# Kernel tuning notes

Measured on AMD Instinct MI355X. Metric: run time of the kernel, lower is better.

## Reference

```python
import jax, jax.numpy as jnp
import numpy as np

IN_FEATURES = 212445
NODE_SIZES = [IN_FEATURES, 65536, 16384, 128]
N_CLASSES = 20
BATCH = 32


def setup_inputs() -> dict:
    key = jax.random.key(0)
    ks = jax.random.split(key, 16)
    inp = {
        "x": jax.random.normal(ks[0], (BATCH, IN_FEATURES), dtype=jnp.float32),
        "W0": jax.random.normal(ks[1], (32, 1), dtype=jnp.float32) * 0.1,
        "b0": jax.random.normal(ks[2], (32,), dtype=jnp.float32) * 0.1,
        "W1": jax.random.normal(ks[3], (64, 32), dtype=jnp.float32) * 0.1,
        "b1": jax.random.normal(ks[4], (64,), dtype=jnp.float32) * 0.1,
        "W2": jax.random.normal(ks[5], (128, 64), dtype=jnp.float32) * 0.1,
        "b2": jax.random.normal(ks[6], (128,), dtype=jnp.float32) * 0.1,
        "fc_w": jax.random.normal(ks[7], (N_CLASSES, 128 * 128), dtype=jnp.float32) * 0.01,
        "fc_b": jax.random.normal(ks[8], (N_CLASSES,), dtype=jnp.float32) * 0.01,
        # random-tree adjacency: each input node has one parent output node
        "parent0": jax.random.randint(ks[9], (NODE_SIZES[0],), 0, NODE_SIZES[1], dtype=jnp.int32),
        "parent1": jax.random.randint(ks[10], (NODE_SIZES[1],), 0, NODE_SIZES[2], dtype=jnp.int32),
        "parent2": jax.random.randint(ks[11], (NODE_SIZES[2],), 0, NODE_SIZES[3], dtype=jnp.int32),
    }
    return inp


def _fgl(z, parent, n_out, W, b):
    """FGL layer: tree-adjacency reduction over nodes + channel mix.
    z: [N, C_in, n_in] -> [N, C_out, n_out]
    """
    N, C, n_in = z.shape
    # segment-sum reduce input nodes into their parent output node
    zt = jnp.moveaxis(z, 2, 0).reshape(n_in, N * C)          # [n_in, N*C]
    s = jax.ops.segment_sum(zt, parent, num_segments=n_out)  # [n_out, N*C]
    s = jnp.moveaxis(s.reshape(n_out, N, C), 0, 2)           # [N, C_in, n_out]
    # channel mixing (weight-normed linear over channels, shared across nodes)
    return jnp.einsum("oc,ncj->noj", W, s) + b[None, :, None]


def reference(x, W0, b0, W1, b1, W2, b2, fc_w, fc_b, parent0, parent1, parent2):
    N = x.shape[0]
    z = x[:, None, :]                                   # [N, 1, in_features]
    z = _fgl(z, parent0, NODE_SIZES[1], W0, b0)         # [N, 32, 65536]
    z = _fgl(z, parent1, NODE_SIZES[2], W1, b1)         # [N, 64, 16384]
    z = _fgl(z, parent2, NODE_SIZES[3], W2, b2)         # [N, 128, 128]
    logits = z.reshape(N, -1) @ fc_w.T + fc_b           # [N, n_classes]
    return logits
```

## Files before the change

### kernel.cpp

```cpp
#include <hip/hip_runtime.h>

#define IN_FEATURES 212445
#define N1 65536
#define N2 16384
#define NCLS 20
#define BATCH 32
#define HIST_BLOCKS 16


__global__ __launch_bounds__(256) void k_setup(
    const float* __restrict__ W0, const float* __restrict__ b0,
    const float* __restrict__ W1, const float* __restrict__ b1,
    const float* __restrict__ W2,
    const int* __restrict__ p1, const int* __restrict__ p2,
    float* __restrict__ t3, int* __restrict__ hist,
    float* __restrict__ u2, float* __restrict__ v2, float* __restrict__ w2)
{
    int t = threadIdx.x;
    int b = blockIdx.x;
    if (b == 0) {
        __shared__ float su1[64], sv1[64];
        if (t < 64) {
            float a = 0.f, bb = 0.f;
            for (int c = 0; c < 32; ++c) {
                float w = W1[t * 32 + c];
                a  += w * W0[c];
                bb += w * b0[c];
            }
            su1[t] = a; sv1[t] = bb;
        }
        __syncthreads();
        if (t < 128) {
            float a = 0.f, bb = 0.f, c = 0.f;
            for (int j = 0; j < 64; ++j) {
                float w = W2[t * 64 + j];
                a  += w * su1[j];
                bb += w * sv1[j];
                c  += w * b1[j];
            }
            u2[t] = a; v2[t] = bb; w2[t] = c;
        }
    } else if (b == 1) {
        for (int s = t; s < BATCH * 128; s += 256) t3[s] = 0.f;
    } else {
        __shared__ int hA[128], hB[128];
        if (t < 128) { hA[t] = 0; hB[t] = 0; }
        __syncthreads();
        const int total = N1 + N2;
        const int stride = HIST_BLOCKS * 256;
        for (int idx = (b - 2) * 256 + t; idx < total; idx += stride) {
            if (idx < N1) atomicAdd(&hA[p2[p1[idx]]], 1);
            else          atomicAdd(&hB[p2[idx - N1]], 1);
        }
        __syncthreads();
        hist[(b - 2) * 256 + t] = (t < 128) ? hA[t] : hB[t - 128];
    }
}

__global__ __launch_bounds__(256) void k_t3(
    const float* __restrict__ x,
    const int* __restrict__ p0, const int* __restrict__ p1,
    const int* __restrict__ p2, float* __restrict__ t3)
{
    __shared__ float acc[BATCH * 128];
    int t = threadIdx.x;
    for (int s = t; s < BATCH * 128; s += 256) acc[s] = 0.f;
    __syncthreads();

    for (int i = blockIdx.x * 256 + t; i < IN_FEATURES; i += 256 * 256) {
        int m = p2[p1[p0[i]]];
        const float* xp = x + i;
        #pragma unroll
        for (int r = 0; r < BATCH; ++r) {
            atomicAdd(&acc[r * 128 + m], xp[r * IN_FEATURES]);
        }
    }
    __syncthreads();
    for (int s = t; s < BATCH * 128; s += 256)
        atomicAdd(&t3[s], acc[s]);
}

__global__ __launch_bounds__(128) void k_final(
    const float* __restrict__ fc_w, const float* __restrict__ fc_b,
    const float* __restrict__ b2,
    const float* __restrict__ u2, const float* __restrict__ v2,
    const float* __restrict__ w2,
    const int* __restrict__ hist, const float* __restrict__ t3,
    float* __restrict__ out)
{
    __shared__ float su[128], sv[128], sw[128], sb[128];
    __shared__ float sA[128], red[128];
    __shared__ float st3[BATCH * 129];
    __shared__ float sconst;
    int m = threadIdx.x;
    int cls = blockIdx.x;

    su[m] = u2[m]; sv[m] = v2[m]; sw[m] = w2[m]; sb[m] = b2[m];
    for (int s = m; s < BATCH * 128; s += 128) {
        int r = s >> 7, mm = s & 127;
        st3[r * 129 + mm] = t3[s];
    }
    int c2 = 0, cn2 = 0;
    #pragma unroll
    for (int h = 0; h < HIST_BLOCKS; ++h) {
        c2  += hist[h * 256 + m];
        cn2 += hist[h * 256 + 128 + m];
    }
    __syncthreads();

    const float* fw = fc_w + cls * 16384 + m;
    float Sa = 0.f, Sv = 0.f, Sw = 0.f, Sb = 0.f;
    #pragma unroll 4
    for (int o = 0; o < 128; ++o) {
        float w = fw[o * 128];
        Sa += w * su[o];
        Sv += w * sv[o];
        Sw += w * sw[o];
        Sb += w * sb[o];
    }
    sA[m] = Sa;
    red[m] = (float)c2 * Sv + (float)cn2 * Sw + Sb;
    __syncthreads();
    for (int s = 64; s > 0; s >>= 1) {
        if (m < s) red[m] += red[m + s];
        __syncthreads();
    }
    if (m == 0) sconst = red[0] + fc_b[cls];
    __syncthreads();

    int n = m >> 2, q = m & 3;
    const float* tr = st3 + n * 129 + q * 32;
    const float* ar = sA + q * 32;
    float s = 0.f;
    #pragma unroll
    for (int k = 0; k < 32; ++k) s += ar[k] * tr[k];
    red[m] = s;
    __syncthreads();
    if (q == 0)
        out[n * NCLS + cls] = sconst + red[m] + red[m + 1] + red[m + 2] + red[m + 3];
}

extern "C" void kernel_launch(void* const* d_in, const int* in_sizes, int n_in,
                              void* d_out, int out_size, void* d_ws, size_t ws_size,
                              hipStream_t stream)
{
    const float* x    = (const float*)d_in[0];
    const float* W0   = (const float*)d_in[1];
    const float* b0   = (const float*)d_in[2];
    const float* W1   = (const float*)d_in[3];
    const float* b1   = (const float*)d_in[4];
    const float* W2   = (const float*)d_in[5];
    const float* b2   = (const float*)d_in[6];
    const float* fc_w = (const float*)d_in[7];
    const float* fc_b = (const float*)d_in[8];
    const int*   p0   = (const int*)d_in[9];
    const int*   p1   = (const int*)d_in[10];
    const int*   p2   = (const int*)d_in[11];

    char* ws = (char*)d_ws;
    float* t3   = (float*)(ws + 0);
    int*   hist = (int*)(ws + 16384);
    float* u2   = (float*)(ws + 32768);
    float* v2   = (float*)(ws + 33280);
    float* w2   = (float*)(ws + 33792);

    k_setup<<<2 + HIST_BLOCKS, 256, 0, stream>>>(W0, b0, W1, b1, W2, p1, p2,
                                                 t3, hist, u2, v2, w2);
    k_t3<<<256, 256, 0, stream>>>(x, p0, p1, p2, t3);
    k_final<<<NCLS, 128, 0, stream>>>(fc_w, fc_b, b2, u2, v2, w2, hist, t3,
                                      (float*)d_out);
}
```

Baseline: 154.9 us.

## Precompute composed parent index and split t3 reduction by row and chunk

```diff
diff --git a/kernel.cpp b/kernel.cpp
--- a/kernel.cpp
+++ b/kernel.cpp
@@ -5,16 +5,22 @@
 #define N2 16384
 #define NCLS 20
 #define BATCH 32
-#define HIST_BLOCKS 16
+#define HIST_BLOCKS 32
+#define MCHUNK 1024
+#define MBLOCKS ((IN_FEATURES + MCHUNK - 1) / MCHUNK)
+#define TCHUNK 4096
+#define TCHUNKS ((IN_FEATURES + TCHUNK - 1) / TCHUNK)
 
 
 __global__ __launch_bounds__(256) void k_setup(
     const float* __restrict__ W0, const float* __restrict__ b0,
     const float* __restrict__ W1, const float* __restrict__ b1,
     const float* __restrict__ W2,
-    const int* __restrict__ p1, const int* __restrict__ p2,
+    const int* __restrict__ p0, const int* __restrict__ p1,
+    const int* __restrict__ p2,
     float* __restrict__ t3, int* __restrict__ hist,
-    float* __restrict__ u2, float* __restrict__ v2, float* __restrict__ w2)
+    float* __restrict__ u2, float* __restrict__ v2, float* __restrict__ w2,
+    int* __restrict__ midx)
 {
     int t = threadIdx.x;
     int b = blockIdx.x;
@@ -42,7 +48,7 @@
         }
     } else if (b == 1) {
         for (int s = t; s < BATCH * 128; s += 256) t3[s] = 0.f;
-    } else {
+    } else if (b < 2 + HIST_BLOCKS) {
         __shared__ int hA[128], hB[128];
         if (t < 128) { hA[t] = 0; hB[t] = 0; }
         __syncthreads();
@@ -54,33 +60,57 @@
         }
         __syncthreads();
         hist[(b - 2) * 256 + t] = (t < 128) ? hA[t] : hB[t - 128];
+    } else {
+        int mb = b - (2 + HIST_BLOCKS);
+        int base = mb * MCHUNK;
+        #pragma unroll
+        for (int u = 0; u < MCHUNK / 256; ++u) {
+            int i = base + u * 256 + t;
+            if (i < IN_FEATURES) midx[i] = p2[p1[p0[i]]];
+        }
     }
 }
 
 __global__ __launch_bounds__(256) void k_t3(
-    const float* __restrict__ x,
-    const int* __restrict__ p0, const int* __restrict__ p1,
-    const int* __restrict__ p2, float* __restrict__ t3)
-{
-    __shared__ float acc[BATCH * 128];
+    const float* __restrict__ x, const int* __restrict__ midx,
+    float* __restrict__ t3)
+{
+    __shared__ float hist[4 * 128];
     int t = threadIdx.x;
-    for (int s = t; s < BATCH * 128; s += 256) acc[s] = 0.f;
-    __syncthreads();
-
-    for (int i = blockIdx.x * 256 + t; i < IN_FEATURES; i += 256 * 256) {
-        int m = p2[p1[p0[i]]];
-        const float* xp = x + i;
-        #pragma unroll
-        for (int r = 0; r < BATCH; ++r) {
-            atomicAdd(&acc[r * 128 + m], xp[r * IN_FEATURES]);
-        }
-    }
-    __syncthreads();
-    for (int s = t; s < BATCH * 128; s += 256)
-        atomicAdd(&t3[s], acc[s]);
-}
-
-__global__ __launch_bounds__(128) void k_final(
+    for (int s = t; s < 512; s += 256) hist[s] = 0.f;
+    __syncthreads();
+
+    int row   = blockIdx.x & 31;
+    int chunk = blockIdx.x >> 5;
+    int base  = chunk * TCHUNK;
+    const float* xr = x + (size_t)row * IN_FEATURES;
+    float* hw = hist + (t >> 6) * 128;
+
+    if (base + TCHUNK <= IN_FEATURES) {
+        for (int k = 0; k < TCHUNK / 1024; ++k) {
+            float v[4]; int mi[4];
+            #pragma unroll
+            for (int u = 0; u < 4; ++u) {
+                int i = base + (k * 4 + u) * 256 + t;
+                v[u]  = xr[i];
+                mi[u] = midx[i];
+            }
+            #pragma unroll
+            for (int u = 0; u < 4; ++u)
+                atomicAdd(&hw[mi[u]], v[u]);
+        }
+    } else {
+        for (int i = base + t; i < IN_FEATURES; i += 256)
+            atomicAdd(&hw[midx[i]], xr[i]);
+    }
+    __syncthreads();
+    if (t < 128) {
+        float s = hist[t] + hist[128 + t] + hist[256 + t] + hist[384 + t];
+        atomicAdd(&t3[row * 128 + t], s);
+    }
+}
+
+__global__ __launch_bounds__(256) void k_final(
     const float* __restrict__ fc_w, const float* __restrict__ fc_b,
     const float* __restrict__ b2,
     const float* __restrict__ u2, const float* __restrict__ v2,
@@ -89,55 +119,63 @@
     float* __restrict__ out)
 {
     __shared__ float su[128], sv[128], sw[128], sb[128];
-    __shared__ float sA[128], red[128];
+    __shared__ float sA[128];
+    __shared__ float pA[256], pV[256], pW[256], pB[256];
+    __shared__ float red[256];
     __shared__ float st3[BATCH * 129];
     __shared__ float sconst;
-    int m = threadIdx.x;
+    int t = threadIdx.x;
+    int m = t & 127, h = t >> 7;
     int cls = blockIdx.x;
 
-    su[m] = u2[m]; sv[m] = v2[m]; sw[m] = w2[m]; sb[m] = b2[m];
-    for (int s = m; s < BATCH * 128; s += 128) {
-        int r = s >> 7, mm = s & 127;
-        st3[r * 129 + mm] = t3[s];
-    }
-    int c2 = 0, cn2 = 0;
-    #pragma unroll
-    for (int h = 0; h < HIST_BLOCKS; ++h) {
-        c2  += hist[h * 256 + m];
-        cn2 += hist[h * 256 + 128 + m];
-    }
+    if (h == 0) { su[m] = u2[m]; sv[m] = v2[m]; sw[m] = w2[m]; sb[m] = b2[m]; }
+    for (int s = t; s < BATCH * 128; s += 256)
+        st3[(s >> 7) * 129 + (s & 127)] = t3[s];
     __syncthreads();
 
     const float* fw = fc_w + cls * 16384 + m;
     float Sa = 0.f, Sv = 0.f, Sw = 0.f, Sb = 0.f;
-    #pragma unroll 4
-    for (int o = 0; o < 128; ++o) {
-        float w = fw[o * 128];
-        Sa += w * su[o];
-        Sv += w * sv[o];
-        Sw += w * sw[o];
-        Sb += w * sb[o];
-    }
-    sA[m] = Sa;
-    red[m] = (float)c2 * Sv + (float)cn2 * Sw + Sb;
-    __syncthreads();
-    for (int s = 64; s > 0; s >>= 1) {
-        if (m < s) red[m] += red[m + s];
-        __syncthreads();
-    }
-    if (m == 0) sconst = red[0] + fc_b[cls];
-    __syncthreads();
-
-    int n = m >> 2, q = m & 3;
-    const float* tr = st3 + n * 129 + q * 32;
-    const float* ar = sA + q * 32;
+    #pragma unroll 8
+    for (int o = h * 64; o < h * 64 + 64; ++o) {
+        float wv = fw[o * 128];
+        Sa += wv * su[o]; Sv += wv * sv[o]; Sw += wv * sw[o]; Sb += wv * sb[o];
+    }
+    pA[t] = Sa; pV[t] = Sv; pW[t] = Sw; pB[t] = Sb;
+    __syncthreads();
+    if (h == 0) {
+        Sa = pA[m] + pA[128 + m]; Sv = pV[m] + pV[128 + m];
+        Sw = pW[m] + pW[128 + m]; Sb = pB[m] + pB[128 + m];
+        int c2 = 0, cn2 = 0;
+        #pragma unroll
+        for (int hb = 0; hb < HIST_BLOCKS; ++hb) {
+            c2  += hist[hb * 256 + m];
+            cn2 += hist[hb * 256 + 128 + m];
+        }
+        sA[m] = Sa;
+        red[m] = (float)c2 * Sv + (float)cn2 * Sw + Sb;
+    }
+    __syncthreads();
+    for (int s2 = 64; s2 > 0; s2 >>= 1) {
+        if (t < s2) red[t] += red[t + s2];
+        __syncthreads();
+    }
+    if (t == 0) sconst = red[0] + fc_b[cls];
+    __syncthreads();
+
+    int n = t >> 3, oc = t & 7;
+    const float* tr = st3 + n * 129 + oc * 16;
+    const float* ar = sA + oc * 16;
     float s = 0.f;
     #pragma unroll
-    for (int k = 0; k < 32; ++k) s += ar[k] * tr[k];
-    red[m] = s;
-    __syncthreads();
-    if (q == 0)
-        out[n * NCLS + cls] = sconst + red[m] + red[m + 1] + red[m + 2] + red[m + 3];
+    for (int k = 0; k < 16; ++k) s += ar[k] * tr[k];
+    red[t] = s;
+    __syncthreads();
+    if (oc == 0) {
+        float tot = sconst;
+        #pragma unroll
+        for (int k = 0; k < 8; ++k) tot += red[t + k];
+        out[n * NCLS + cls] = tot;
+    }
 }
 
 extern "C" void kernel_launch(void* const* d_in, const int* in_sizes, int n_in,
@@ -160,13 +198,14 @@
     char* ws = (char*)d_ws;
     float* t3   = (float*)(ws + 0);
     int*   hist = (int*)(ws + 16384);
-    float* u2   = (float*)(ws + 32768);
-    float* v2   = (float*)(ws + 33280);
-    float* w2   = (float*)(ws + 33792);
-
-    k_setup<<<2 + HIST_BLOCKS, 256, 0, stream>>>(W0, b0, W1, b1, W2, p1, p2,
-                                                 t3, hist, u2, v2, w2);
-    k_t3<<<256, 256, 0, stream>>>(x, p0, p1, p2, t3);
-    k_final<<<NCLS, 128, 0, stream>>>(fc_w, fc_b, b2, u2, v2, w2, hist, t3,
+    float* u2   = (float*)(ws + 49152);
+    float* v2   = (float*)(ws + 49664);
+    float* w2   = (float*)(ws + 50176);
+    int*   midx = (int*)(ws + 51200);
+
+    k_setup<<<2 + HIST_BLOCKS + MBLOCKS, 256, 0, stream>>>(
+        W0, b0, W1, b1, W2, p0, p1, p2, t3, hist, u2, v2, w2, midx);
+    k_t3<<<BATCH * TCHUNKS, 256, 0, stream>>>(x, midx, t3);
+    k_final<<<NCLS, 256, 0, stream>>>(fc_w, fc_b, b2, u2, v2, w2, hist, t3,
                                       (float*)d_out);
 }
```

After: 136.6 us. 11.8% less time.

## Precompute composed leaf-to-root index map and fuse final reduction into main kernel

Applied to the files above, without the earlier changes.

```diff
diff --git a/kernel.cpp b/kernel.cpp
--- a/kernel.cpp
+++ b/kernel.cpp
@@ -1,143 +1,224 @@
 #include <hip/hip_runtime.h>
 
-#define IN_FEATURES 212445
+#define IF 212445
 #define N1 65536
 #define N2 16384
 #define NCLS 20
 #define BATCH 32
-#define HIST_BLOCKS 16
-
+#define HISTB 32
+#define MCHUNK 1024
+#define MBLK ((IF + MCHUNK - 1) / MCHUNK)
+#define TCHUNK 2048
+#define NCH ((IF + TCHUNK - 1) / TCHUNK)
+#define TOTALB (8 * NCH)
+
+#define OFF_T3   0
+#define OFF_DONE 16384
+#define OFF_HIST 16400
+#define OFF_A    49168
+#define OFF_SV   59408
+#define OFF_SW   69648
+#define OFF_CP   79888
+#define OFF_MIDX 79968
 
 __global__ __launch_bounds__(256) void k_setup(
     const float* __restrict__ W0, const float* __restrict__ b0,
     const float* __restrict__ W1, const float* __restrict__ b1,
-    const float* __restrict__ W2,
-    const int* __restrict__ p1, const int* __restrict__ p2,
-    float* __restrict__ t3, int* __restrict__ hist,
-    float* __restrict__ u2, float* __restrict__ v2, float* __restrict__ w2)
+    const float* __restrict__ W2, const float* __restrict__ b2,
+    const float* __restrict__ fc_w, const float* __restrict__ fc_b,
+    const int* __restrict__ p0, const int* __restrict__ p1,
+    const int* __restrict__ p2, char* __restrict__ ws)
 {
-    int t = threadIdx.x;
-    int b = blockIdx.x;
-    if (b == 0) {
+    int t = threadIdx.x, b = blockIdx.x;
+    float* t3   = (float*)(ws + OFF_T3);
+    int*   done = (int*)(ws + OFF_DONE);
+    int*   hist = (int*)(ws + OFF_HIST);
+    float* A    = (float*)(ws + OFF_A);
+    float* Sv   = (float*)(ws + OFF_SV);
+    float* Sw   = (float*)(ws + OFF_SW);
+    float* CP   = (float*)(ws + OFF_CP);
+    int*   midx = (int*)(ws + OFF_MIDX);
+
+    if (b < MBLK) {
+        int i = b * MCHUNK + 4 * t;
+        if (i + 3 < IF) {
+            int4 p = *(const int4*)(p0 + i);
+            int4 r;
+            r.x = p2[p1[p.x]]; r.y = p2[p1[p.y]];
+            r.z = p2[p1[p.z]]; r.w = p2[p1[p.w]];
+            *(int4*)(midx + i) = r;
+        } else {
+            for (int j = i; j < IF; ++j) midx[j] = p2[p1[p0[j]]];
+        }
+    } else if (b == MBLK) {
+        for (int s = t; s < BATCH * 128; s += 256) t3[s] = 0.f;
+        if (t == 0) *done = 0;
+    } else if (b < MBLK + 1 + HISTB) {
+        int hb = b - (MBLK + 1);
+        __shared__ int hA[128], hB[128];
+        if (t < 128) { hA[t] = 0; hB[t] = 0; }
+        __syncthreads();
+        const int total = N1 + N2;
+        for (int idx = hb * 256 + t; idx < total; idx += HISTB * 256) {
+            if (idx < N1) atomicAdd(&hA[p2[p1[idx]]], 1);
+            else          atomicAdd(&hB[p2[idx - N1]], 1);
+        }
+        __syncthreads();
+        hist[hb * 256 + t] = (t < 128) ? hA[t] : hB[t - 128];
+    } else {
+        int cls = b - (MBLK + 1 + HISTB);
         __shared__ float su1[64], sv1[64];
+        __shared__ float su2[128], sv2[128], sw2[128], sb2[128];
+        __shared__ float pA[256], pV[256], pW[256], pB[256];
         if (t < 64) {
             float a = 0.f, bb = 0.f;
             for (int c = 0; c < 32; ++c) {
                 float w = W1[t * 32 + c];
-                a  += w * W0[c];
-                bb += w * b0[c];
+                a += w * W0[c]; bb += w * b0[c];
             }
             su1[t] = a; sv1[t] = bb;
         }
+        if (t >= 128) sb2[t - 128] = b2[t - 128];
         __syncthreads();
         if (t < 128) {
             float a = 0.f, bb = 0.f, c = 0.f;
             for (int j = 0; j < 64; ++j) {
                 float w = W2[t * 64 + j];
-                a  += w * su1[j];
-                bb += w * sv1[j];
-                c  += w * b1[j];
+                a += w * su1[j]; bb += w * sv1[j]; c += w * b1[j];
             }
-            u2[t] = a; v2[t] = bb; w2[t] = c;
-        }
-    } else if (b == 1) {
-        for (int s = t; s < BATCH * 128; s += 256) t3[s] = 0.f;
-    } else {
-        __shared__ int hA[128], hB[128];
-        if (t < 128) { hA[t] = 0; hB[t] = 0; }
-        __syncthreads();
-        const int total = N1 + N2;
-        const int stride = HIST_BLOCKS * 256;
-        for (int idx = (b - 2) * 256 + t; idx < total; idx += stride) {
-            if (idx < N1) atomicAdd(&hA[p2[p1[idx]]], 1);
-            else          atomicAdd(&hB[p2[idx - N1]], 1);
-        }
-        __syncthreads();
-        hist[(b - 2) * 256 + t] = (t < 128) ? hA[t] : hB[t - 128];
+            su2[t] = a; sv2[t] = bb; sw2[t] = c;
+        }
+        __syncthreads();
+        int m = t & 127, h = t >> 7;
+        const float* fw = fc_w + cls * 16384 + m;
+        float Sa = 0.f, SvA = 0.f, SwA = 0.f, SbA = 0.f;
+        #pragma unroll 8
+        for (int o = h * 64; o < h * 64 + 64; ++o) {
+            float w = fw[o * 128];
+            Sa += w * su2[o]; SvA += w * sv2[o];
+            SwA += w * sw2[o]; SbA += w * sb2[o];
+        }
+        pA[t] = Sa; pV[t] = SvA; pW[t] = SwA; pB[t] = SbA;
+        __syncthreads();
+        if (t < 128) {
+            A [cls * 128 + t] = pA[t] + pA[t + 128];
+            Sv[cls * 128 + t] = pV[t] + pV[t + 128];
+            Sw[cls * 128 + t] = pW[t] + pW[t + 128];
+            pB[t] = pB[t] + pB[t + 128];
+        }
+        __syncthreads();
+        for (int s2 = 64; s2 > 0; s2 >>= 1) {
+            if (t < s2) pB[t] += pB[t + s2];
+            __syncthreads();
+        }
+        if (t == 0) CP[cls] = fc_b[cls] + pB[0];
     }
 }
 
-__global__ __launch_bounds__(256) void k_t3(
-    const float* __restrict__ x,
-    const int* __restrict__ p0, const int* __restrict__ p1,
-    const int* __restrict__ p2, float* __restrict__ t3)
-{
-    __shared__ float acc[BATCH * 128];
-    int t = threadIdx.x;
-    for (int s = t; s < BATCH * 128; s += 256) acc[s] = 0.f;
-    __syncthreads();
-
-    for (int i = blockIdx.x * 256 + t; i < IN_FEATURES; i += 256 * 256) {
-        int m = p2[p1[p0[i]]];
-        const float* xp = x + i;
-        #pragma unroll
-        for (int r = 0; r < BATCH; ++r) {
-            atomicAdd(&acc[r * 128 + m], xp[r * IN_FEATURES]);
-        }
-    }
-    __syncthreads();
-    for (int s = t; s < BATCH * 128; s += 256)
-        atomicAdd(&t3[s], acc[s]);
-}
-
-__global__ __launch_bounds__(128) void k_final(
-    const float* __restrict__ fc_w, const float* __restrict__ fc_b,
-    const float* __restrict__ b2,
-    const float* __restrict__ u2, const float* __restrict__ v2,
-    const float* __restrict__ w2,
-    const int* __restrict__ hist, const float* __restrict__ t3,
+__global__ __launch_bounds__(256) void k_main(
+    const float* __restrict__ x, char* __restrict__ ws,
     float* __restrict__ out)
 {
-    __shared__ float su[128], sv[128], sw[128], sb[128];
-    __shared__ float sA[128], red[128];
-    __shared__ float st3[BATCH * 129];
-    __shared__ float sconst;
-    int m = threadIdx.x;
-    int cls = blockIdx.x;
-
-    su[m] = u2[m]; sv[m] = v2[m]; sw[m] = w2[m]; sb[m] = b2[m];
-    for (int s = m; s < BATCH * 128; s += 128) {
-        int r = s >> 7, mm = s & 127;
-        st3[r * 129 + mm] = t3[s];
-    }
-    int c2 = 0, cn2 = 0;
+    __shared__ float smem[8192];
+    __shared__ int isLast;
+    int t = threadIdx.x;
+    float* t3   = (float*)(ws + OFF_T3);
+    int*   done = (int*)(ws + OFF_DONE);
+    const int*   hist = (const int*)(ws + OFF_HIST);
+    const float* A    = (const float*)(ws + OFF_A);
+    const float* Svt  = (const float*)(ws + OFF_SV);
+    const float* Swt  = (const float*)(ws + OFF_SW);
+    const float* CP   = (const float*)(ws + OFF_CP);
+    const int*   midx = (const int*)(ws + OFF_MIDX);
+
+    for (int s = t; s < 512; s += 256) smem[s] = 0.f;
+    __syncthreads();
+
+    int g = blockIdx.x & 7, chunk = blockIdx.x >> 3;
+    int r0 = g * 4, base = chunk * TCHUNK;
+    const float* x0 = x + (size_t)(r0 + 0) * IF;
+    const float* x1 = x + (size_t)(r0 + 1) * IF;
+    const float* x2 = x + (size_t)(r0 + 2) * IF;
+    const float* x3 = x + (size_t)(r0 + 3) * IF;
+    int iend = base + TCHUNK; if (iend > IF) iend = IF;
+
+    #pragma unroll 2
+    for (int i = base + t; i < iend; i += 256) {
+        int m = midx[i];
+        float v0 = x0[i], v1 = x1[i], v2 = x2[i], v3 = x3[i];
+        atomicAdd(&smem[      m], v0);
+        atomicAdd(&smem[128 + m], v1);
+        atomicAdd(&smem[256 + m], v2);
+        atomicAdd(&smem[384 + m], v3);
+    }
+    __syncthreads();
+    {
+        int s0 = t, s1 = t + 256;
+        atomicAdd(&t3[(r0 + (s0 >> 7)) * 128 + (s0 & 127)], smem[s0]);
+        atomicAdd(&t3[(r0 + (s1 >> 7)) * 128 + (s1 & 127)], smem[s1]);
+    }
+    __threadfence();
+    if (t == 0) isLast = (atomicAdd(done, 1) == TOTALB - 1) ? 1 : 0;
+    __syncthreads();
+    if (!isLast) return;
+    __threadfence();
+
+    float* st3   = smem;
+    float* sA    = smem + 4224;
+    float* c2f   = smem + 6784;
+    float* cnf   = smem + 6912;
+    float* cpart = smem + 7040;
+    float* scst  = smem + 7200;
+
     #pragma unroll
-    for (int h = 0; h < HIST_BLOCKS; ++h) {
-        c2  += hist[h * 256 + m];
-        cn2 += hist[h * 256 + 128 + m];
-    }
-    __syncthreads();
-
-    const float* fw = fc_w + cls * 16384 + m;
-    float Sa = 0.f, Sv = 0.f, Sw = 0.f, Sb = 0.f;
-    #pragma unroll 4
-    for (int o = 0; o < 128; ++o) {
-        float w = fw[o * 128];
-        Sa += w * su[o];
-        Sv += w * sv[o];
-        Sw += w * sw[o];
-        Sb += w * sb[o];
-    }
-    sA[m] = Sa;
-    red[m] = (float)c2 * Sv + (float)cn2 * Sw + Sb;
-    __syncthreads();
-    for (int s = 64; s > 0; s >>= 1) {
-        if (m < s) red[m] += red[m + s];
-        __syncthreads();
-    }
-    if (m == 0) sconst = red[0] + fc_b[cls];
-    __syncthreads();
-
-    int n = m >> 2, q = m & 3;
-    const float* tr = st3 + n * 129 + q * 32;
-    const float* ar = sA + q * 32;
-    float s = 0.f;
+    for (int k = 0; k < 16; ++k) {
+        int s = t + 256 * k;
+        float v = __hip_atomic_load(&t3[s], __ATOMIC_RELAXED,
+                                    __HIP_MEMORY_SCOPE_AGENT);
+        st3[(s & 127) * 33 + (s >> 7)] = v;
+    }
     #pragma unroll
-    for (int k = 0; k < 32; ++k) s += ar[k] * tr[k];
-    red[m] = s;
-    __syncthreads();
-    if (q == 0)
-        out[n * NCLS + cls] = sconst + red[m] + red[m + 1] + red[m + 2] + red[m + 3];
+    for (int k = 0; k < 10; ++k) {
+        int q = t + 256 * k;
+        sA[(q & 127) * 20 + (q >> 7)] = A[q];
+    }
+    {
+        int acc = 0;
+        #pragma unroll
+        for (int h = 0; h < HISTB; ++h) acc += hist[h * 256 + t];
+        if (t < 128) c2f[t] = (float)acc; else cnf[t - 128] = (float)acc;
+    }
+    __syncthreads();
+    if (t < 160) {
+        int cls = t >> 3, m0 = (t & 7) * 16;
+        const float* sv = Svt + cls * 128;
+        const float* sw = Swt + cls * 128;
+        float s = 0.f;
+        #pragma unroll
+        for (int m = m0; m < m0 + 16; ++m)
+            s += c2f[m] * sv[m] + cnf[m] * sw[m];
+        cpart[t] = s;
+    }
+    __syncthreads();
+    if (t < NCLS) {
+        float s = CP[t];
+        #pragma unroll
+        for (int k = 0; k < 8; ++k) s += cpart[t * 8 + k];
+        scst[t] = s;
+    }
+    __syncthreads();
+    #pragma unroll
+    for (int k = 0; k < 3; ++k) {
+        int p = t + 256 * k;
+        if (p < BATCH * NCLS) {
+            int n = p / NCLS, cls = p - n * NCLS;
+            float acc = scst[cls];
+            #pragma unroll 8
+            for (int m = 0; m < 128; ++m)
+                acc += sA[m * 20 + cls] * st3[m * 33 + n];
+            out[p] = acc;
+        }
+    }
 }
 
 extern "C" void kernel_launch(void* const* d_in, const int* in_sizes, int n_in,
@@ -157,16 +238,7 @@
     const int*   p1   = (const int*)d_in[10];
     const int*   p2   = (const int*)d_in[11];
 
-    char* ws = (char*)d_ws;
-    float* t3   = (float*)(ws + 0);
-    int*   hist = (int*)(ws + 16384);
-    float* u2   = (float*)(ws + 32768);
-    float* v2   = (float*)(ws + 33280);
-    float* w2   = (float*)(ws + 33792);
-
-    k_setup<<<2 + HIST_BLOCKS, 256, 0, stream>>>(W0, b0, W1, b1, W2, p1, p2,
-                                                 t3, hist, u2, v2, w2);
-    k_t3<<<256, 256, 0, stream>>>(x, p0, p1, p2, t3);
-    k_final<<<NCLS, 128, 0, stream>>>(fc_w, fc_b, b2, u2, v2, w2, hist, t3,
-                                      (float*)d_out);
+    k_setup<<<MBLK + 1 + HISTB + NCLS, 256, 0, stream>>>(
+        W0, b0, W1, b1, W2, b2, fc_w, fc_b, p0, p1, p2, (char*)d_ws);
+    k_main<<<TOTALB, 256, 0, stream>>>(x, (char*)d_ws, (float*)d_out);
 }
```

New measurement: 191.0 us. 1.23x slower.
